# Kernel tuning notes

Hardware: AMD Instinct MI355X
Metric: run time of the kernel (lower is better)

Reference implementation:

```python
import jax, jax.numpy as jnp
import numpy as np

N_HEADS = 16
D_HEAD = 64
MAX_POS = 128

def setup_inputs() -> dict:
    key = jax.random.key(0)
    ks = jax.random.split(key, 9)
    B, L, D = 4, 1024, 1024
    s = 0.02
    return {
        'x': jax.random.normal(ks[0], (B, L, D), jnp.float32),
        'pad_mask': jnp.ones((B, L), jnp.float32),
        'Wq': jax.random.normal(ks[1], (D, D), jnp.float32) * s,
        'bq': jnp.zeros((D,), jnp.float32),
        'Wk': jax.random.normal(ks[2], (D, D), jnp.float32) * s,
        'bk': jnp.zeros((D,), jnp.float32),
        'Wv': jax.random.normal(ks[3], (D, D), jnp.float32) * s,
        'bv': jnp.zeros((D,), jnp.float32),
        'Wo': jax.random.normal(ks[4], (D, D), jnp.float32) * s,
        'bo': jnp.zeros((D,), jnp.float32),
        'posK': jax.random.normal(ks[5], (2 * MAX_POS + 1, D_HEAD), jnp.float32) * s,
        'posV': jax.random.normal(ks[6], (2 * MAX_POS + 1, D_HEAD), jnp.float32) * s,
    }

def reference(x, pad_mask, Wq, bq, Wk, bk, Wv, bv, Wo, bo, posK, posV):
    B, L, _ = x.shape
    H, d = N_HEADS, D_HEAD
    def proj(W, b):
        y = x @ W + b                      # [B, L, H*d]
        return y.reshape(B, L, H, d).transpose(0, 2, 1, 3)  # [B, H, L, d]
    Q = proj(Wq, bq)
    K = proj(Wk, bk)
    V = proj(Wv, bv)
    # relative position index, clamped to [-MAX_POS, MAX_POS], shifted to [0, 2*MAX_POS]
    idx = jnp.arange(L)
    pos_index = jnp.clip(idx[None, :] - idx[:, None], -MAX_POS, MAX_POS) + MAX_POS  # [L, L]
    pos_emb_K = posK[pos_index]            # [L, L, d]
    pos_emb_V = posV[pos_index]            # [L, L, d]
    S1 = jnp.einsum('bhqd,bhkd->bhqk', Q, K)
    S2 = jnp.einsum('bhqd,qkd->bhqk', Q, pos_emb_K)
    S = (S1 + S2) / np.sqrt(d).astype(np.float32)
    # NOTE: original multiplies scores by the pad mask (not additive -inf)
    S = S * pad_mask[:, None, None, :]
    A = jax.nn.softmax(S, axis=-1)
    O1 = jnp.einsum('bhqk,bhkd->bhqd', A, V)
    O2 = jnp.einsum('bhqk,qkd->bhqd', A, pos_emb_V)
    out = (O1 + O2).transpose(0, 2, 1, 3).reshape(B, L, H * d)
    return out @ Wo + bo
```

## Files before the change

kernel.cpp:

```cpp
#include <hip/hip_runtime.h>
#include <math.h>

#define L_SEQ 1024
#define NB 4
#define NH 16
#define DH 64
#define BH_TOT (NB * NH)
#define GQ_TOT (BH_TOT * L_SEQ)
#define NPOS 257
#define QP_STRIDE 260
#define LDK 72
#define LDQP 72
#define LDPV 264

typedef unsigned short ushort_t;
typedef __attribute__((ext_vector_type(8))) short bf16x8;
typedef __attribute__((ext_vector_type(4))) float f32x4;

__device__ inline ushort_t f2bf_rne(float x) {
    unsigned u = __float_as_uint(x);
    unsigned r = u + 0x7FFFu + ((u >> 16) & 1u);
    return (ushort_t)(r >> 16);
}
__device__ inline float bf2f(ushort_t h) {
    return __uint_as_float(((unsigned)h) << 16);
}
__device__ inline void split8(float4 a0, float4 a1, uint4* H, uint4* L) {
    float v[8] = {a0.x, a0.y, a0.z, a0.w, a1.x, a1.y, a1.z, a1.w};
    unsigned hh[4], ll[4];
    #pragma unroll
    for (int j = 0; j < 4; j++) {
        ushort_t h0 = f2bf_rne(v[2*j]),   h1 = f2bf_rne(v[2*j+1]);
        ushort_t l0 = f2bf_rne(v[2*j]   - bf2f(h0));
        ushort_t l1 = f2bf_rne(v[2*j+1] - bf2f(h1));
        hh[j] = (unsigned)h0 | ((unsigned)h1 << 16);
        ll[j] = (unsigned)l0 | ((unsigned)l1 << 16);
    }
    *H = (uint4){hh[0], hh[1], hh[2], hh[3]};
    *L = (uint4){ll[0], ll[1], ll[2], ll[3]};
}
__device__ inline uint4 pack8hi(float4 a0, float4 a1) {
    float v[8] = {a0.x, a0.y, a0.z, a0.w, a1.x, a1.y, a1.z, a1.w};
    unsigned hh[4];
    #pragma unroll
    for (int j = 0; j < 4; j++)
        hh[j] = (unsigned)f2bf_rne(v[2*j]) | ((unsigned)f2bf_rne(v[2*j+1]) << 16);
    return (uint4){hh[0], hh[1], hh[2], hh[3]};
}

__global__ __launch_bounds__(256)
void split_f32(const float* __restrict__ A, ushort_t* __restrict__ hi,
               ushort_t* __restrict__ lo)
{
    const size_t base = ((size_t)blockIdx.x * 256 + threadIdx.x) * 8;
    uint4 H, L;
    split8(*(const float4*)(A + base), *(const float4*)(A + base + 4), &H, &L);
    *(uint4*)(hi + base) = H;
    *(uint4*)(lo + base) = L;
}

__global__ __launch_bounds__(256)
void split_transpose(const float* __restrict__ W, ushort_t* __restrict__ Thi,
                     ushort_t* __restrict__ Tlo, int Kdim, int Ndim)
{
    __shared__ float Ws[64][65];
    const int tid = threadIdx.x;
    const int k0 = blockIdx.x * 64;
    const int n0 = blockIdx.y * 64;
    const int r  = tid >> 4;
    const int c4 = (tid & 15) * 4;
    #pragma unroll
    for (int i = 0; i < 4; i++) {
        float4 v = *(const float4*)(W + (size_t)(k0 + r + i*16) * Ndim + n0 + c4);
        Ws[r + i*16][c4+0] = v.x;
        Ws[r + i*16][c4+1] = v.y;
        Ws[r + i*16][c4+2] = v.z;
        Ws[r + i*16][c4+3] = v.w;
    }
    __syncthreads();
    #pragma unroll
    for (int i = 0; i < 4; i++) {
        const int nl = r + i*16;
        ushort_t h[4], l[4];
        #pragma unroll
        for (int j = 0; j < 4; j++) {
            float x = Ws[c4 + j][nl];
            h[j] = f2bf_rne(x);
            l[j] = f2bf_rne(x - bf2f(h[j]));
        }
        size_t off = (size_t)(n0 + nl) * Kdim + k0 + c4;
        uint2 H, L;
        H.x = (unsigned)h[0] | ((unsigned)h[1] << 16);
        H.y = (unsigned)h[2] | ((unsigned)h[3] << 16);
        L.x = (unsigned)l[0] | ((unsigned)l[1] << 16);
        L.y = (unsigned)l[2] | ((unsigned)l[3] << 16);
        *(uint2*)(Thi + off) = H;
        *(uint2*)(Tlo + off) = L;
    }
}

__global__ __launch_bounds__(256)
void prep_pvt(const float* __restrict__ posV, ushort_t* __restrict__ pvTg)
{
    __shared__ float Ws[64][65];
    const int tid = threadIdx.x;
    const int c = blockIdx.x;
    {
        const int r  = tid >> 2;
        const int d0 = (tid & 3) * 16;
        const float* src = posV + (size_t)(c * 64 + r + 1) * 64 + d0;
        #pragma unroll
        for (int i = 0; i < 4; i++) {
            float4 v = *(const float4*)(src + i * 4);
            Ws[r][d0 + i*4 + 0] = v.x;
            Ws[r][d0 + i*4 + 1] = v.y;
            Ws[r][d0 + i*4 + 2] = v.z;
            Ws[r][d0 + i*4 + 3] = v.w;
        }
    }
    __syncthreads();
    {
        const int d  = tid >> 2;
        const int r0 = (tid & 3) * 16;
        #pragma unroll
        for (int k = 0; k < 16; k++)
            pvTg[(size_t)d * LDPV + c * 64 + r0 + k] = f2bf_rne(Ws[r0 + k][d]);
    }
}

__global__ __launch_bounds__(256)
void gemm_mfma(const ushort_t* __restrict__ Ahi, const ushort_t* __restrict__ Alo,
               const ushort_t* __restrict__ Bhi, const ushort_t* __restrict__ Blo,
               const float* __restrict__ bias, float* __restrict__ C,
               int M, int N, int K, int mode)
{
    __shared__ ushort_t As[2][64 * LDK];
    __shared__ ushort_t Bs[2][64 * LDK];
    const int tid  = threadIdx.x;
    const int m0   = blockIdx.x * 64;
    const int n0   = blockIdx.y * 64;
    const int wave = tid >> 6;
    const int lane = tid & 63;
    const int w0 = wave >> 1;
    const int w1 = wave & 1;
    const int lr = lane & 15;
    const int lq = lane >> 4;

    f32x4 acc[2][2];
    #pragma unroll
    for (int i = 0; i < 2; i++)
        #pragma unroll
        for (int j = 0; j < 2; j++)
            acc[i][j] = (f32x4){0.f, 0.f, 0.f, 0.f};

    for (int k0 = 0; k0 < K; k0 += 64) {
        __syncthreads();
        #pragma unroll
        for (int c = 0; c < 2; c++) {
            const int n   = c * 256 + tid;
            const int row = n >> 3;
            const int col = (n & 7) * 8;
            const size_t ga = (size_t)(m0 + row) * K + k0 + col;
            const size_t gb = (size_t)(n0 + row) * K + k0 + col;
            const int la = row * LDK + col;
            *(uint4*)&As[0][la] = *(const uint4*)(Ahi + ga);
            *(uint4*)&As[1][la] = *(const uint4*)(Alo + ga);
            *(uint4*)&Bs[0][la] = *(const uint4*)(Bhi + gb);
            *(uint4*)&Bs[1][la] = *(const uint4*)(Blo + gb);
        }
        __syncthreads();
        #pragma unroll
        for (int ks = 0; ks < 2; ks++) {
            bf16x8 ah[2], al[2], bh[2], bl[2];
            #pragma unroll
            for (int i = 0; i < 2; i++) {
                const int ar = (w0*32 + i*16 + lr) * LDK + ks*32 + lq*8;
                ah[i] = *(const bf16x8*)&As[0][ar];
                al[i] = *(const bf16x8*)&As[1][ar];
                const int br = (w1*32 + i*16 + lr) * LDK + ks*32 + lq*8;
                bh[i] = *(const bf16x8*)&Bs[0][br];
                bl[i] = *(const bf16x8*)&Bs[1][br];
            }
            #pragma unroll
            for (int i = 0; i < 2; i++)
                #pragma unroll
                for (int j = 0; j < 2; j++) {
                    acc[i][j] = __builtin_amdgcn_mfma_f32_16x16x32_bf16(ah[i], bh[j], acc[i][j], 0, 0, 0);
                    acc[i][j] = __builtin_amdgcn_mfma_f32_16x16x32_bf16(ah[i], bl[j], acc[i][j], 0, 0, 0);
                    acc[i][j] = __builtin_amdgcn_mfma_f32_16x16x32_bf16(al[i], bh[j], acc[i][j], 0, 0, 0);
                }
        }
    }

    #pragma unroll
    for (int j = 0; j < 2; j++) {
        const int colg = n0 + w1*32 + j*16 + lr;
        const float bcol = bias[colg];
        #pragma unroll
        for (int i = 0; i < 2; i++) {
            #pragma unroll
            for (int r = 0; r < 4; r++) {
                const int m = m0 + w0*32 + i*16 + lq*4 + r;
                const float v = acc[i][j][r] + bcol;
                if (mode == 0) {
                    C[(size_t)m * N + colg] = v;
                } else if (mode == 1) {
                    const int b = m >> 10, lp = m & 1023;
                    const int h = colg >> 6, dd = colg & 63;
                    C[((size_t)(b * NH + h) * L_SEQ + lp) * DH + dd] = v;
                } else {
                    const int b = m >> 10, lp = m & 1023;
                    const int h = colg >> 6, dd = colg & 63;
                    C[((size_t)(b * NH + h) * DH + dd) * L_SEQ + lp] = v;
                }
            }
        }
    }
}

__global__ __launch_bounds__(256)
void qp_kernel(const float* __restrict__ Q, const float* __restrict__ posK,
               ushort_t* __restrict__ Qpu)
{
    __shared__ float Qt[64 * 64];
    __shared__ float Pt[64 * 64];
    const int tid = threadIdx.x;
    const size_t gq0 = (size_t)blockIdx.x * 64;
    const int ty = tid >> 4;
    const int tx = tid & 15;

    {
        const int q  = tid >> 2;
        const int d0 = (tid & 3) * 16;
        const float* qrow = Q + (gq0 + q) * DH + d0;
        #pragma unroll
        for (int i = 0; i < 4; i++) {
            float4 v = *(const float4*)(qrow + i * 4);
            Qt[(d0 + i*4 + 0) * 64 + q] = v.x;
            Qt[(d0 + i*4 + 1) * 64 + q] = v.y;
            Qt[(d0 + i*4 + 2) * 64 + q] = v.z;
            Qt[(d0 + i*4 + 3) * 64 + q] = v.w;
        }
    }

    for (int c = 0; c < 4; c++) {
        __syncthreads();
        {
            const int r  = tid >> 2;
            const int d0 = (tid & 3) * 16;
            const float* krow = posK + (size_t)(c * 64 + r) * DH + d0;
            #pragma unroll
            for (int i = 0; i < 4; i++) {
                float4 v = *(const float4*)(krow + i * 4);
                Pt[(d0 + i*4 + 0) * 64 + r] = v.x;
                Pt[(d0 + i*4 + 1) * 64 + r] = v.y;
                Pt[(d0 + i*4 + 2) * 64 + r] = v.z;
                Pt[(d0 + i*4 + 3) * 64 + r] = v.w;
            }
        }
        __syncthreads();

        float acc[16];
        #pragma unroll
        for (int i = 0; i < 16; i++) acc[i] = 0.f;
        #pragma unroll 16
        for (int d = 0; d < 64; d++) {
            float4 qv = *(const float4*)&Qt[d * 64 + ty * 4];
            float4 pv = *(const float4*)&Pt[d * 64 + tx * 4];
            float qa[4] = {qv.x, qv.y, qv.z, qv.w};
            float pa[4] = {pv.x, pv.y, pv.z, pv.w};
            #pragma unroll
            for (int i = 0; i < 4; i++)
                #pragma unroll
                for (int j = 0; j < 4; j++)
                    acc[i * 4 + j] += qa[i] * pa[j];
        }
        #pragma unroll
        for (int i = 0; i < 4; i++) {
            uint2 o;
            o.x = (unsigned)f2bf_rne(acc[i*4+0]) | ((unsigned)f2bf_rne(acc[i*4+1]) << 16);
            o.y = (unsigned)f2bf_rne(acc[i*4+2]) | ((unsigned)f2bf_rne(acc[i*4+3]) << 16);
            *(uint2*)(Qpu + (gq0 + ty * 4 + i) * QP_STRIDE + c * 64 + tx * 4) = o;
        }
    }

    __syncthreads();
    if (tid < 64) {
        float s = 0.f;
        #pragma unroll 16
        for (int d = 0; d < 64; d++)
            s += Qt[d * 64 + tid] * posK[256 * 64 + d];
        Qpu[(gq0 + tid) * QP_STRIDE + 256] = f2bf_rne(s);
    }
}

__global__ __launch_bounds__(256)
void attn_kernel(const float* __restrict__ Q, const float* __restrict__ K,
                 const float* __restrict__ Vt, const ushort_t* __restrict__ Qpu,
                 const float* __restrict__ pm,
                 ushort_t* __restrict__ SbandU,
                 float* __restrict__ O1a, float* __restrict__ O1b,
                 float* __restrict__ lsum2, float* __restrict__ clo2,
                 float* __restrict__ chi2)
{
    __shared__ ushort_t Ks[64 * LDK];
    __shared__ ushort_t Vs[64 * LDK];
    __shared__ ushort_t QpsP[64 * LDQP];
    __shared__ float mk[64];

    const int tid = threadIdx.x;
    const int blk = blockIdx.x;
    const int bh  = blk >> 5;
    const int qb  = (blk >> 1) & 15;
    const int ks  = blk & 1;
    const int b   = bh >> 4;
    const int q0  = qb * 64;
    const size_t gq0 = (size_t)bh * L_SEQ + q0;
    const int wave = tid >> 6, lane = tid & 63;
    const int lr = lane & 15, lq = lane >> 4;
    const int qw = wave * 16;

    const int sr0 = tid >> 3,          sc0 = (tid & 7) * 8;
    const int sr1 = (256 + tid) >> 3,  sc1 = ((256 + tid) & 7) * 8;
    const int qpRowL = qw + (lane >> 2);
    const int qpCol0 = (lane & 3) * 16;

    const float* Kg  = K  + (size_t)bh * (L_SEQ * DH);
    const float* Vtg = Vt + (size_t)bh * (DH * L_SEQ);

    bf16x8 qa[2];
    {
        const float* qrow = Q + (gq0 + qw + lr) * DH;
        #pragma unroll
        for (int kc = 0; kc < 2; kc++) {
            const float* s = qrow + kc * 32 + lq * 8;
            uint4 u = pack8hi(*(const float4*)s, *(const float4*)(s + 4));
            qa[kc] = *(bf16x8*)&u;
        }
    }

    if (ks == 0 && tid < 64) {
        const int q = q0 + tid;
        ushort_t* bandRow = SbandU + (gq0 + tid) * 256;
        for (int j = 0; j < 127 - q; j++)    bandRow[j] = 0;
        for (int j = 254; j > 1150 - q; j--) bandRow[j] = 0;
        bandRow[255] = 0;
    }

    f32x4 Oacc[4];
    #pragma unroll
    for (int j = 0; j < 4; j++) Oacc[j] = (f32x4){0.f, 0.f, 0.f, 0.f};
    float lpart[4] = {}, clpart[4] = {}, chpart[4] = {};

    float4 kva[2][2], kvb[2][2];
    ushort_t qpr[16];
    float mkr = 0.f;
    {
        const int k0 = ks * 512;
        const float* ka0 = Kg + (size_t)(k0 + sr0) * DH + sc0;
        const float* ka1 = Kg + (size_t)(k0 + sr1) * DH + sc1;
        kva[0][0] = *(const float4*)ka0;      kva[0][1] = *(const float4*)(ka0 + 4);
        kva[1][0] = *(const float4*)ka1;      kva[1][1] = *(const float4*)(ka1 + 4);
        const float* va0 = Vtg + (size_t)sr0 * L_SEQ + k0 + sc0;
        const float* va1 = Vtg + (size_t)sr1 * L_SEQ + k0 + sc1;
        kvb[0][0] = *(const float4*)va0;      kvb[0][1] = *(const float4*)(va0 + 4);
        kvb[1][0] = *(const float4*)va1;      kvb[1][1] = *(const float4*)(va1 + 4);
        const int qg = q0 + qpRowL;
        #pragma unroll
        for (int c = 0; c < 16; c++) {
            int rel = k0 + qpCol0 + c - qg;
            rel = rel < -128 ? -128 : (rel > 128 ? 128 : rel);
            qpr[c] = Qpu[(gq0 + qpRowL) * QP_STRIDE + rel + 128];
        }
        if (tid < 64) mkr = pm[b * L_SEQ + k0 + tid];
    }

    for (int t = 0; t < 8; t++) {
        const int k0 = (ks * 8 + t) * 64;
        __syncthreads();

        *(uint4*)&Ks[sr0 * LDK + sc0] = pack8hi(kva[0][0], kva[0][1]);
        *(uint4*)&Ks[sr1 * LDK + sc1] = pack8hi(kva[1][0], kva[1][1]);
        *(uint4*)&Vs[sr0 * LDK + sc0] = pack8hi(kvb[0][0], kvb[0][1]);
        *(uint4*)&Vs[sr1 * LDK + sc1] = pack8hi(kvb[1][0], kvb[1][1]);
        {
            ushort_t* dst = &QpsP[qpRowL * LDQP + qpCol0];
            #pragma unroll
            for (int c = 0; c < 8; c++)
                ((unsigned*)dst)[c] = (unsigned)qpr[2*c] | ((unsigned)qpr[2*c+1] << 16);
        }
        if (tid < 64) mk[tid] = mkr;
        __syncthreads();

        if (t < 7) {
            const int k0n = k0 + 64;
            const float* ka0 = Kg + (size_t)(k0n + sr0) * DH + sc0;
            const float* ka1 = Kg + (size_t)(k0n + sr1) * DH + sc1;
            kva[0][0] = *(const float4*)ka0;  kva[0][1] = *(const float4*)(ka0 + 4);
            kva[1][0] = *(const float4*)ka1;  kva[1][1] = *(const float4*)(ka1 + 4);
            const float* va0 = Vtg + (size_t)sr0 * L_SEQ + k0n + sc0;
            const float* va1 = Vtg + (size_t)sr1 * L_SEQ + k0n + sc1;
            kvb[0][0] = *(const float4*)va0;  kvb[0][1] = *(const float4*)(va0 + 4);
            kvb[1][0] = *(const float4*)va1;  kvb[1][1] = *(const float4*)(va1 + 4);
            const int qg = q0 + qpRowL;
            #pragma unroll
            for (int c = 0; c < 16; c++) {
                int rel = k0n + qpCol0 + c - qg;
                rel = rel < -128 ? -128 : (rel > 128 ? 128 : rel);
                qpr[c] = Qpu[(gq0 + qpRowL) * QP_STRIDE + rel + 128];
            }
            if (tid < 64) mkr = pm[b * L_SEQ + k0n + tid];
        }

        f32x4 Sacc[4];
        #pragma unroll
        for (int j = 0; j < 4; j++) Sacc[j] = (f32x4){0.f, 0.f, 0.f, 0.f};
        #pragma unroll
        for (int kc = 0; kc < 2; kc++) {
            #pragma unroll
            for (int j = 0; j < 4; j++) {
                bf16x8 kb = *(const bf16x8*)&Ks[(j*16 + lr) * LDK + kc*32 + lq*8];
                Sacc[j] = __builtin_amdgcn_mfma_f32_16x16x32_bf16(qa[kc], kb, Sacc[j], 0, 0, 0);
            }
        }

        ushort_t pb[4][4];
        #pragma unroll
        for (int r = 0; r < 4; r++) {
            const int ql = qw + lq*4 + r;
            const int q  = q0 + ql;
            const size_t gq = gq0 + ql;
            ushort_t* bandRow = SbandU + gq * 256 + 127;
            #pragma unroll
            for (int j = 0; j < 4; j++) {
                const int kl = j*16 + lr;
                const int k  = k0 + kl;
                const int rel = k - q;
                float s = (Sacc[j][r] + bf2f(QpsP[ql * LDQP + kl])) * 0.125f;
                s *= mk[kl];
                const float p = __expf(s);
                lpart[r] += p;
                const ushort_t ph = f2bf_rne(p);
                if (rel <= -128)      clpart[r] += p;
                else if (rel >= 128)  chpart[r] += p;
                else                  bandRow[rel] = ph;
                pb[j][r] = ph;
            }
        }

        #pragma unroll
        for (int r = 0; r < 4; r++)
            #pragma unroll
            for (int j = 0; j < 4; j++)
                QpsP[(qw + lq*4 + r) * LDQP + j*16 + lr] = pb[j][r];

        #pragma unroll
        for (int kc = 0; kc < 2; kc++) {
            bf16x8 pa = *(const bf16x8*)&QpsP[(qw + lr) * LDQP + kc*32 + lq*8];
            #pragma unroll
            for (int j = 0; j < 4; j++) {
                bf16x8 vb = *(const bf16x8*)&Vs[(j*16 + lr) * LDK + kc*32 + lq*8];
                Oacc[j] = __builtin_amdgcn_mfma_f32_16x16x32_bf16(pa, vb, Oacc[j], 0, 0, 0);
            }
        }
    }

    #pragma unroll
    for (int off = 1; off < 16; off <<= 1) {
        #pragma unroll
        for (int r = 0; r < 4; r++) {
            lpart[r]  += __shfl_xor(lpart[r],  off, 64);
            clpart[r] += __shfl_xor(clpart[r], off, 64);
            chpart[r] += __shfl_xor(chpart[r], off, 64);
        }
    }
    if (lr == 0) {
        #pragma unroll
        for (int r = 0; r < 4; r++) {
            const size_t o = (size_t)ks * GQ_TOT + gq0 + qw + lq*4 + r;
            lsum2[o] = lpart[r];
            clo2[o]  = clpart[r];
            chi2[o]  = chpart[r];
        }
    }

    float* O1o = ks ? O1b : O1a;
    #pragma unroll
    for (int j = 0; j < 4; j++)
        #pragma unroll
        for (int r = 0; r < 4; r++)
            O1o[(gq0 + qw + lq*4 + r) * DH + j*16 + lr] = Oacc[j][r];
}

__global__ __launch_bounds__(256)
void post_mfma(const ushort_t* __restrict__ SbandU, const ushort_t* __restrict__ pvTg,
               const float* __restrict__ O1a, const float* __restrict__ O1b,
               const float* __restrict__ lsum2, const float* __restrict__ clo2,
               const float* __restrict__ chi2, const float* __restrict__ posV,
               ushort_t* __restrict__ athi, ushort_t* __restrict__ atlo)
{
    __shared__ ushort_t pvT[64 * LDPV];
    const int tid = threadIdx.x;
    const size_t q0 = (size_t)blockIdx.x * 64;
    const int wave = tid >> 6, lane = tid & 63;
    const int w0 = wave >> 1, w1 = wave & 1;
    const int lr = lane & 15, lq = lane >> 4;

    {
        const unsigned* src = (const unsigned*)pvTg;
        unsigned* dst = (unsigned*)pvT;
        for (int i = tid; i < 64 * LDPV / 2; i += 256) dst[i] = src[i];
    }
    __syncthreads();

    f32x4 acc[2][2];
    #pragma unroll
    for (int i = 0; i < 2; i++)
        #pragma unroll
        for (int j = 0; j < 2; j++)
            acc[i][j] = (f32x4){0.f, 0.f, 0.f, 0.f};

    const ushort_t* bandB = SbandU + q0 * 256;
    #pragma unroll
    for (int kc = 0; kc < 8; kc++) {
        bf16x8 a[2], bv[2];
        #pragma unroll
        for (int i = 0; i < 2; i++) {
            a[i]  = *(const bf16x8*)&bandB[(size_t)(w0*32 + i*16 + lr) * 256 + kc*32 + lq*8];
            bv[i] = *(const bf16x8*)&pvT[(w1*32 + i*16 + lr) * LDPV + kc*32 + lq*8];
        }
        #pragma unroll
        for (int i = 0; i < 2; i++)
            #pragma unroll
            for (int j = 0; j < 2; j++)
                acc[i][j] = __builtin_amdgcn_mfma_f32_16x16x32_bf16(a[i], bv[j], acc[i][j], 0, 0, 0);
    }

    #pragma unroll
    for (int i = 0; i < 2; i++) {
        #pragma unroll
        for (int r = 0; r < 4; r++) {
            const int ql = w0*32 + i*16 + lq*4 + r;
            const size_t gq = q0 + ql;
            const float li = lsum2[gq] + lsum2[GQ_TOT + gq];
            const float cl = clo2[gq]  + clo2[GQ_TOT + gq];
            const float ch = chi2[gq]  + chi2[GQ_TOT + gq];
            const float inv = 1.0f / li;
            const int b  = (int)(gq >> 14);
            const int h  = (int)((gq >> 10) & 15);
            const int lp = (int)(gq & 1023);
            const size_t obase = ((size_t)(b * L_SEQ + lp) * 1024) + h * 64;
            #pragma unroll
            for (int j = 0; j < 2; j++) {
                const int dd = w1*32 + j*16 + lr;
                float o = O1a[gq * DH + dd] + O1b[gq * DH + dd] + acc[i][j][r]
                        + cl * posV[dd] + ch * posV[256 * 64 + dd];
                o *= inv;
                const ushort_t hh = f2bf_rne(o);
                const ushort_t ll = f2bf_rne(o - bf2f(hh));
                athi[obase + dd] = hh;
                atlo[obase + dd] = ll;
            }
        }
    }
}

extern "C" void kernel_launch(void* const* d_in, const int* in_sizes, int n_in,
                              void* d_out, int out_size, void* d_ws, size_t ws_size,
                              hipStream_t stream)
{
    const float* x    = (const float*)d_in[0];
    const float* pmk  = (const float*)d_in[1];
    const float* Wq   = (const float*)d_in[2];
    const float* bq   = (const float*)d_in[3];
    const float* Wk   = (const float*)d_in[4];
    const float* bk   = (const float*)d_in[5];
    const float* Wv   = (const float*)d_in[6];
    const float* bv   = (const float*)d_in[7];
    const float* Wo   = (const float*)d_in[8];
    const float* bo   = (const float*)d_in[9];
    const float* posK = (const float*)d_in[10];
    const float* posV = (const float*)d_in[11];
    float* out = (float*)d_out;

    float* ws = (float*)d_ws;
    float* Qb = ws;
    float* Kb = Qb + (size_t)GQ_TOT * DH;
    float* Vb = Kb + (size_t)GQ_TOT * DH;
    ushort_t* Qpu    = (ushort_t*)(Vb + (size_t)GQ_TOT * DH);
    ushort_t* SbandU = Qpu + (size_t)GQ_TOT * QP_STRIDE;
    ushort_t* athi   = SbandU + (size_t)GQ_TOT * 256;
    ushort_t* atlo   = athi + (size_t)GQ_TOT * DH;
    ushort_t* pvTg   = atlo + (size_t)GQ_TOT * DH;
    float* O1a   = (float*)(pvTg + 64 * LDPV);
    float* O1b   = O1a   + (size_t)GQ_TOT * DH;
    float* lsum2 = O1b   + (size_t)GQ_TOT * DH;
    float* clo2  = lsum2 + 2 * (size_t)GQ_TOT;
    float* chi2  = clo2  + 2 * (size_t)GQ_TOT;

    ushort_t* bb  = SbandU;
    ushort_t* xhi = bb;
    ushort_t* xlo = xhi + 4194304;
    ushort_t* wqh = xlo + 4194304;
    ushort_t* wql = wqh + 1048576;
    ushort_t* wkh = wql + 1048576;
    ushort_t* wkl = wkh + 1048576;
    ushort_t* wvh = wkl + 1048576;
    ushort_t* wvl = wvh + 1048576;
    ushort_t* woh = bb;
    ushort_t* wol = woh + 1048576;

    dim3 tg(16, 16), gg(64, 16), gb(256);

    split_f32<<<dim3(2048), gb, 0, stream>>>(x, xhi, xlo);
    split_transpose<<<tg, gb, 0, stream>>>(Wq, wqh, wql, 1024, 1024);
    split_transpose<<<tg, gb, 0, stream>>>(Wk, wkh, wkl, 1024, 1024);
    split_transpose<<<tg, gb, 0, stream>>>(Wv, wvh, wvl, 1024, 1024);
    prep_pvt<<<dim3(4), gb, 0, stream>>>(posV, pvTg);
    gemm_mfma<<<gg, gb, 0, stream>>>(xhi, xlo, wqh, wql, bq, Qb, 4096, 1024, 1024, 1);
    gemm_mfma<<<gg, gb, 0, stream>>>(xhi, xlo, wkh, wkl, bk, Kb, 4096, 1024, 1024, 1);
    gemm_mfma<<<gg, gb, 0, stream>>>(xhi, xlo, wvh, wvl, bv, Vb, 4096, 1024, 1024, 2);
    qp_kernel<<<dim3(GQ_TOT / 64), gb, 0, stream>>>(Qb, posK, Qpu);
    attn_kernel<<<dim3(2048), gb, 0, stream>>>(Qb, Kb, Vb, Qpu, pmk,
                                               SbandU, O1a, O1b, lsum2, clo2, chi2);
    post_mfma<<<dim3(GQ_TOT / 64), gb, 0, stream>>>(SbandU, pvTg, O1a, O1b, lsum2,
                                                    clo2, chi2, posV, athi, atlo);
    split_transpose<<<tg, gb, 0, stream>>>(Wo, woh, wol, 1024, 1024);
    gemm_mfma<<<gg, gb, 0, stream>>>(athi, atlo, woh, wol, bo, out, 4096, 1024, 1024, 0);
}
```

Measured before the change: 447.4 us.

## Drop x low-part split term and emit K/V projections directly as bf16

The QKV projections now use only the bf16 high part of x (two MFMA terms instead of three), so the x low split is neither computed nor loaded. The K and V projection GEMMs write bf16 directly, which halves their stores and lets the attention kernel load bf16 tiles without converting them in registers. The output projection keeps the three-term path. Accuracy of Q/K/V drops because the x low-order residual is discarded, and the nterms branch adds a runtime check inside the GEMM loop.

New measurement: 419.4 us. -6.3%, faster.

```diff
diff --git a/kernel.cpp b/kernel.cpp
--- a/kernel.cpp
+++ b/kernel.cpp
@@ -49,14 +49,11 @@
 }
 
 __global__ __launch_bounds__(256)
-void split_f32(const float* __restrict__ A, ushort_t* __restrict__ hi,
-               ushort_t* __restrict__ lo)
+void split_f32_hi(const float* __restrict__ A, ushort_t* __restrict__ hi)
 {
     const size_t base = ((size_t)blockIdx.x * 256 + threadIdx.x) * 8;
-    uint4 H, L;
-    split8(*(const float4*)(A + base), *(const float4*)(A + base + 4), &H, &L);
-    *(uint4*)(hi + base) = H;
-    *(uint4*)(lo + base) = L;
+    *(uint4*)(hi + base) =
+        pack8hi(*(const float4*)(A + base), *(const float4*)(A + base + 4));
 }
 
 __global__ __launch_bounds__(256)
@@ -131,8 +128,8 @@
 __global__ __launch_bounds__(256)
 void gemm_mfma(const ushort_t* __restrict__ Ahi, const ushort_t* __restrict__ Alo,
                const ushort_t* __restrict__ Bhi, const ushort_t* __restrict__ Blo,
-               const float* __restrict__ bias, float* __restrict__ C,
-               int M, int N, int K, int mode)
+               const float* __restrict__ bias, void* __restrict__ Cout,
+               int M, int N, int K, int mode, int nterms)
 {
     __shared__ ushort_t As[2][64 * LDK];
     __shared__ ushort_t Bs[2][64 * LDK];
@@ -164,19 +161,19 @@
             const size_t gb = (size_t)(n0 + row) * K + k0 + col;
             const int la = row * LDK + col;
             *(uint4*)&As[0][la] = *(const uint4*)(Ahi + ga);
-            *(uint4*)&As[1][la] = *(const uint4*)(Alo + ga);
+            if (nterms == 3)
+                *(uint4*)&As[1][la] = *(const uint4*)(Alo + ga);
             *(uint4*)&Bs[0][la] = *(const uint4*)(Bhi + gb);
             *(uint4*)&Bs[1][la] = *(const uint4*)(Blo + gb);
         }
         __syncthreads();
         #pragma unroll
         for (int ks = 0; ks < 2; ks++) {
-            bf16x8 ah[2], al[2], bh[2], bl[2];
+            bf16x8 ah[2], bh[2], bl[2];
             #pragma unroll
             for (int i = 0; i < 2; i++) {
                 const int ar = (w0*32 + i*16 + lr) * LDK + ks*32 + lq*8;
                 ah[i] = *(const bf16x8*)&As[0][ar];
-                al[i] = *(const bf16x8*)&As[1][ar];
                 const int br = (w1*32 + i*16 + lr) * LDK + ks*32 + lq*8;
                 bh[i] = *(const bf16x8*)&Bs[0][br];
                 bl[i] = *(const bf16x8*)&Bs[1][br];
@@ -187,8 +184,18 @@
                 for (int j = 0; j < 2; j++) {
                     acc[i][j] = __builtin_amdgcn_mfma_f32_16x16x32_bf16(ah[i], bh[j], acc[i][j], 0, 0, 0);
                     acc[i][j] = __builtin_amdgcn_mfma_f32_16x16x32_bf16(ah[i], bl[j], acc[i][j], 0, 0, 0);
-                    acc[i][j] = __builtin_amdgcn_mfma_f32_16x16x32_bf16(al[i], bh[j], acc[i][j], 0, 0, 0);
                 }
+            if (nterms == 3) {
+                bf16x8 al[2];
+                #pragma unroll
+                for (int i = 0; i < 2; i++)
+                    al[i] = *(const bf16x8*)&As[1][(w0*32 + i*16 + lr) * LDK + ks*32 + lq*8];
+                #pragma unroll
+                for (int i = 0; i < 2; i++)
+                    #pragma unroll
+                    for (int j = 0; j < 2; j++)
+                        acc[i][j] = __builtin_amdgcn_mfma_f32_16x16x32_bf16(al[i], bh[j], acc[i][j], 0, 0, 0);
+            }
         }
     }
 
@@ -203,15 +210,19 @@
                 const int m = m0 + w0*32 + i*16 + lq*4 + r;
                 const float v = acc[i][j][r] + bcol;
                 if (mode == 0) {
-                    C[(size_t)m * N + colg] = v;
+                    ((float*)Cout)[(size_t)m * N + colg] = v;
                 } else if (mode == 1) {
                     const int b = m >> 10, lp = m & 1023;
                     const int h = colg >> 6, dd = colg & 63;
-                    C[((size_t)(b * NH + h) * L_SEQ + lp) * DH + dd] = v;
+                    ((float*)Cout)[((size_t)(b * NH + h) * L_SEQ + lp) * DH + dd] = v;
+                } else if (mode == 2) {
+                    const int b = m >> 10, lp = m & 1023;
+                    const int h = colg >> 6, dd = colg & 63;
+                    ((ushort_t*)Cout)[((size_t)(b * NH + h) * L_SEQ + lp) * DH + dd] = f2bf_rne(v);
                 } else {
                     const int b = m >> 10, lp = m & 1023;
                     const int h = colg >> 6, dd = colg & 63;
-                    C[((size_t)(b * NH + h) * DH + dd) * L_SEQ + lp] = v;
+                    ((ushort_t*)Cout)[((size_t)(b * NH + h) * DH + dd) * L_SEQ + lp] = f2bf_rne(v);
                 }
             }
         }
@@ -295,8 +306,8 @@
 }
 
 __global__ __launch_bounds__(256)
-void attn_kernel(const float* __restrict__ Q, const float* __restrict__ K,
-                 const float* __restrict__ Vt, const ushort_t* __restrict__ Qpu,
+void attn_kernel(const float* __restrict__ Q, const ushort_t* __restrict__ Ku,
+                 const ushort_t* __restrict__ Vtu, const ushort_t* __restrict__ Qpu,
                  const float* __restrict__ pm,
                  ushort_t* __restrict__ SbandU,
                  float* __restrict__ O1a, float* __restrict__ O1b,
@@ -325,8 +336,8 @@
     const int qpRowL = qw + (lane >> 2);
     const int qpCol0 = (lane & 3) * 16;
 
-    const float* Kg  = K  + (size_t)bh * (L_SEQ * DH);
-    const float* Vtg = Vt + (size_t)bh * (DH * L_SEQ);
+    const ushort_t* Kg  = Ku  + (size_t)bh * (L_SEQ * DH);
+    const ushort_t* Vtg = Vtu + (size_t)bh * (DH * L_SEQ);
 
     bf16x8 qa[2];
     {
@@ -352,19 +363,15 @@
     for (int j = 0; j < 4; j++) Oacc[j] = (f32x4){0.f, 0.f, 0.f, 0.f};
     float lpart[4] = {}, clpart[4] = {}, chpart[4] = {};
 
-    float4 kva[2][2], kvb[2][2];
+    uint4 kva0, kva1, kvb0, kvb1;
     ushort_t qpr[16];
     float mkr = 0.f;
     {
         const int k0 = ks * 512;
-        const float* ka0 = Kg + (size_t)(k0 + sr0) * DH + sc0;
-        const float* ka1 = Kg + (size_t)(k0 + sr1) * DH + sc1;
-        kva[0][0] = *(const float4*)ka0;      kva[0][1] = *(const float4*)(ka0 + 4);
-        kva[1][0] = *(const float4*)ka1;      kva[1][1] = *(const float4*)(ka1 + 4);
-        const float* va0 = Vtg + (size_t)sr0 * L_SEQ + k0 + sc0;
-        const float* va1 = Vtg + (size_t)sr1 * L_SEQ + k0 + sc1;
-        kvb[0][0] = *(const float4*)va0;      kvb[0][1] = *(const float4*)(va0 + 4);
-        kvb[1][0] = *(const float4*)va1;      kvb[1][1] = *(const float4*)(va1 + 4);
+        kva0 = *(const uint4*)(Kg + (size_t)(k0 + sr0) * DH + sc0);
+        kva1 = *(const uint4*)(Kg + (size_t)(k0 + sr1) * DH + sc1);
+        kvb0 = *(const uint4*)(Vtg + (size_t)sr0 * L_SEQ + k0 + sc0);
+        kvb1 = *(const uint4*)(Vtg + (size_t)sr1 * L_SEQ + k0 + sc1);
         const int qg = q0 + qpRowL;
         #pragma unroll
         for (int c = 0; c < 16; c++) {
@@ -379,10 +386,10 @@
         const int k0 = (ks * 8 + t) * 64;
         __syncthreads();
 
-        *(uint4*)&Ks[sr0 * LDK + sc0] = pack8hi(kva[0][0], kva[0][1]);
-        *(uint4*)&Ks[sr1 * LDK + sc1] = pack8hi(kva[1][0], kva[1][1]);
-        *(uint4*)&Vs[sr0 * LDK + sc0] = pack8hi(kvb[0][0], kvb[0][1]);
-        *(uint4*)&Vs[sr1 * LDK + sc1] = pack8hi(kvb[1][0], kvb[1][1]);
+        *(uint4*)&Ks[sr0 * LDK + sc0] = kva0;
+        *(uint4*)&Ks[sr1 * LDK + sc1] = kva1;
+        *(uint4*)&Vs[sr0 * LDK + sc0] = kvb0;
+        *(uint4*)&Vs[sr1 * LDK + sc1] = kvb1;
         {
             ushort_t* dst = &QpsP[qpRowL * LDQP + qpCol0];
             #pragma unroll
@@ -394,14 +401,10 @@
 
         if (t < 7) {
             const int k0n = k0 + 64;
-            const float* ka0 = Kg + (size_t)(k0n + sr0) * DH + sc0;
-            const float* ka1 = Kg + (size_t)(k0n + sr1) * DH + sc1;
-            kva[0][0] = *(const float4*)ka0;  kva[0][1] = *(const float4*)(ka0 + 4);
-            kva[1][0] = *(const float4*)ka1;  kva[1][1] = *(const float4*)(ka1 + 4);
-            const float* va0 = Vtg + (size_t)sr0 * L_SEQ + k0n + sc0;
-            const float* va1 = Vtg + (size_t)sr1 * L_SEQ + k0n + sc1;
-            kvb[0][0] = *(const float4*)va0;  kvb[0][1] = *(const float4*)(va0 + 4);
-            kvb[1][0] = *(const float4*)va1;  kvb[1][1] = *(const float4*)(va1 + 4);
+            kva0 = *(const uint4*)(Kg + (size_t)(k0n + sr0) * DH + sc0);
+            kva1 = *(const uint4*)(Kg + (size_t)(k0n + sr1) * DH + sc1);
+            kvb0 = *(const uint4*)(Vtg + (size_t)sr0 * L_SEQ + k0n + sc0);
+            kvb1 = *(const uint4*)(Vtg + (size_t)sr1 * L_SEQ + k0n + sc1);
             const int qg = q0 + qpRowL;
             #pragma unroll
             for (int c = 0; c < 16; c++) {
@@ -585,13 +588,13 @@
 
     float* ws = (float*)d_ws;
     float* Qb = ws;
-    float* Kb = Qb + (size_t)GQ_TOT * DH;
-    float* Vb = Kb + (size_t)GQ_TOT * DH;
-    ushort_t* Qpu    = (ushort_t*)(Vb + (size_t)GQ_TOT * DH);
+    ushort_t* Kbu = (ushort_t*)(Qb + (size_t)GQ_TOT * DH);
+    ushort_t* Vtu = Kbu + (size_t)GQ_TOT * DH;
+    ushort_t* Qpu = Vtu + (size_t)GQ_TOT * DH;
     ushort_t* SbandU = Qpu + (size_t)GQ_TOT * QP_STRIDE;
-    ushort_t* athi   = SbandU + (size_t)GQ_TOT * 256;
-    ushort_t* atlo   = athi + (size_t)GQ_TOT * DH;
-    ushort_t* pvTg   = atlo + (size_t)GQ_TOT * DH;
+    ushort_t* athi = SbandU + (size_t)GQ_TOT * 256;
+    ushort_t* atlo = athi + (size_t)GQ_TOT * DH;
+    ushort_t* pvTg = atlo + (size_t)GQ_TOT * DH;
     float* O1a   = (float*)(pvTg + 64 * LDPV);
     float* O1b   = O1a   + (size_t)GQ_TOT * DH;
     float* lsum2 = O1b   + (size_t)GQ_TOT * DH;
@@ -600,8 +603,7 @@
 
     ushort_t* bb  = SbandU;
     ushort_t* xhi = bb;
-    ushort_t* xlo = xhi + 4194304;
-    ushort_t* wqh = xlo + 4194304;
+    ushort_t* wqh = xhi + 4194304;
     ushort_t* wql = wqh + 1048576;
     ushort_t* wkh = wql + 1048576;
     ushort_t* wkl = wkh + 1048576;
@@ -612,19 +614,19 @@
 
     dim3 tg(16, 16), gg(64, 16), gb(256);
 
-    split_f32<<<dim3(2048), gb, 0, stream>>>(x, xhi, xlo);
+    split_f32_hi<<<dim3(2048), gb, 0, stream>>>(x, xhi);
     split_transpose<<<tg, gb, 0, stream>>>(Wq, wqh, wql, 1024, 1024);
     split_transpose<<<tg, gb, 0, stream>>>(Wk, wkh, wkl, 1024, 1024);
     split_transpose<<<tg, gb, 0, stream>>>(Wv, wvh, wvl, 1024, 1024);
     prep_pvt<<<dim3(4), gb, 0, stream>>>(posV, pvTg);
-    gemm_mfma<<<gg, gb, 0, stream>>>(xhi, xlo, wqh, wql, bq, Qb, 4096, 1024, 1024, 1);
-    gemm_mfma<<<gg, gb, 0, stream>>>(xhi, xlo, wkh, wkl, bk, Kb, 4096, 1024, 1024, 1);
-    gemm_mfma<<<gg, gb, 0, stream>>>(xhi, xlo, wvh, wvl, bv, Vb, 4096, 1024, 1024, 2);
+    gemm_mfma<<<gg, gb, 0, stream>>>(xhi, xhi, wqh, wql, bq, Qb,  4096, 1024, 1024, 1, 2);
+    gemm_mfma<<<gg, gb, 0, stream>>>(xhi, xhi, wkh, wkl, bk, Kbu, 4096, 1024, 1024, 2, 2);
+    gemm_mfma<<<gg, gb, 0, stream>>>(xhi, xhi, wvh, wvl, bv, Vtu, 4096, 1024, 1024, 3, 2);
     qp_kernel<<<dim3(GQ_TOT / 64), gb, 0, stream>>>(Qb, posK, Qpu);
-    attn_kernel<<<dim3(2048), gb, 0, stream>>>(Qb, Kb, Vb, Qpu, pmk,
+    attn_kernel<<<dim3(2048), gb, 0, stream>>>(Qb, Kbu, Vtu, Qpu, pmk,
                                                SbandU, O1a, O1b, lsum2, clo2, chi2);
     post_mfma<<<dim3(GQ_TOT / 64), gb, 0, stream>>>(SbandU, pvTg, O1a, O1b, lsum2,
                                                     clo2, chi2, posV, athi, atlo);
     split_transpose<<<tg, gb, 0, stream>>>(Wo, woh, wol, 1024, 1024);
-    gemm_mfma<<<gg, gb, 0, stream>>>(athi, atlo, woh, wol, bo, out, 4096, 1024, 1024, 0);
-}
+    gemm_mfma<<<gg, gb, 0, stream>>>(athi, atlo, woh, wol, bo, out, 4096, 1024, 1024, 0, 3);
+}
```
